# Kernel optimization log

Hardware: AMD Instinct MI355X
Metric: run time of the kernel (lower is better)

## Reference

```python
import jax, jax.numpy as jnp
import numpy as np

HIDDEN = 4096
N_HEADS = 32
N_KV_HEADS = 8
HEAD_DIM = HIDDEN // N_HEADS  # 128
N_GROUPS = N_HEADS // N_KV_HEADS  # 4
ROPE_THETA = 10000.0
NEG_INF = -1e9


def fake_quant(x):
    """Symmetric per-tensor int8 fake quantization (quantize -> dequantize)."""
    scale = jnp.maximum(jnp.max(jnp.abs(x)) / 127.0, 1e-8)
    return jnp.clip(jnp.round(x / scale), -127.0, 127.0) * scale


def q_linear(x, W):
    # torch Linear: y = x @ W.T ; both operands fake-quantized (dequant-inline GEMM)
    return jnp.einsum('bsh,oh->bso', fake_quant(x), fake_quant(W))


def rope_cos_sin(position_ids, head_dim, dtype):
    inv_freq = 1.0 / (ROPE_THETA ** (jnp.arange(0, head_dim, 2, dtype=jnp.float32) / head_dim))
    freqs = position_ids.astype(jnp.float32)[..., None] * inv_freq  # [b, s, hd/2]
    emb = jnp.concatenate([freqs, freqs], axis=-1)                   # [b, s, hd]
    return jnp.cos(emb).astype(dtype), jnp.sin(emb).astype(dtype)


def rotate_half(x):
    x1, x2 = jnp.split(x, 2, axis=-1)
    return jnp.concatenate([-x2, x1], axis=-1)


def setup_inputs() -> dict:
    key = jax.random.key(0)
    ks = jax.random.split(key, 6)
    b, s = 2, 1024
    hidden_states = jax.random.normal(ks[0], (b, s, HIDDEN), dtype=jnp.float32)
    # additive causal mask [b, 1, q, kv]
    causal = jnp.where(jnp.tril(jnp.ones((s, s), dtype=bool)), 0.0, NEG_INF).astype(jnp.float32)
    attention_mask = jnp.broadcast_to(causal[None, None], (b, 1, s, s))
    position_ids = jnp.broadcast_to(jnp.arange(s, dtype=jnp.int64)[None, :], (b, s))
    winit = 1.0 / np.sqrt(HIDDEN)
    Wq = jax.random.normal(ks[1], (HIDDEN, HIDDEN), dtype=jnp.float32) * winit
    Wk = jax.random.normal(ks[2], (N_KV_HEADS * HEAD_DIM, HIDDEN), dtype=jnp.float32) * winit
    Wv = jax.random.normal(ks[3], (N_KV_HEADS * HEAD_DIM, HIDDEN), dtype=jnp.float32) * winit
    Wo = jax.random.normal(ks[4], (HIDDEN, HIDDEN), dtype=jnp.float32) * winit
    return {"hidden_states": hidden_states, "attention_mask": attention_mask,
            "position_ids": position_ids, "Wq": Wq, "Wk": Wk, "Wv": Wv, "Wo": Wo}


def reference(hidden_states, attention_mask, position_ids, Wq, Wk, Wv, Wo):
    b, s, _ = hidden_states.shape
    dtype = hidden_states.dtype

    # quantized QKV projections
    q = q_linear(hidden_states, Wq).reshape(b, s, N_HEADS, HEAD_DIM).transpose(0, 2, 1, 3)
    k = q_linear(hidden_states, Wk).reshape(b, s, N_KV_HEADS, HEAD_DIM).transpose(0, 2, 1, 3)
    v = q_linear(hidden_states, Wv).reshape(b, s, N_KV_HEADS, HEAD_DIM).transpose(0, 2, 1, 3)

    # RoPE
    cos, sin = rope_cos_sin(position_ids, HEAD_DIM, dtype)  # [b, s, hd]
    cos, sin = cos[:, None], sin[:, None]                   # broadcast over heads
    q = q * cos + rotate_half(q) * sin
    k = k * cos + rotate_half(k) * sin

    # GQA: repeat kv heads
    k = jnp.repeat(k, N_GROUPS, axis=1)  # [b, H, s, hd]
    v = jnp.repeat(v, N_GROUPS, axis=1)

    # quantized QK^T (per-tensor fake quant on both operands)
    attn = jnp.einsum('bhqd,bhkd->bhqk', fake_quant(q), fake_quant(k)) / jnp.sqrt(
        jnp.asarray(HEAD_DIM, dtype=jnp.float32)).astype(dtype)
    attn = attn + attention_mask
    attn = jax.nn.softmax(attn.astype(jnp.float32), axis=-1).astype(dtype)
    # attention_dropout = 0.0 (inference)

    # quantized AV matmul
    out = jnp.einsum('bhqk,bhkd->bhqd', fake_quant(attn), fake_quant(v))
    out = out.transpose(0, 2, 1, 3).reshape(b, s, HIDDEN)
    out = q_linear(out, Wo)
    return out
```

## Files before the change

kernel.cpp:

```cpp
#include <hip/hip_runtime.h>
#include <math.h>

#define B_ 2
#define S_ 1024
#define HID 4096
#define NH 32
#define NKV 8
#define HD 128
#define LOG2E 1.44269504088896340736f

typedef short s16x8 __attribute__((ext_vector_type(8)));
typedef float f32x4 __attribute__((ext_vector_type(4)));
typedef unsigned short u16;
typedef u16 u16x4 __attribute__((ext_vector_type(4)));

__device__ __forceinline__ f32x4 mfma16(s16x8 a, s16x8 b, f32x4 c) {
  return __builtin_amdgcn_mfma_f32_16x16x32_bf16(a, b, c, 0, 0, 0);
}
__device__ __forceinline__ u16 f2bf(float f) {
  union { float f; unsigned u; } v; v.f = f;
  return (u16)(v.u >> 16);
}
__device__ __forceinline__ float get_scale(const unsigned* sc, int slot) {
  return fmaxf(__uint_as_float(sc[slot]) / 127.0f, 1e-8f);
}
__device__ __forceinline__ void gload16(const void* g, void* l) {
  __builtin_amdgcn_global_load_lds(
      (const __attribute__((address_space(1))) unsigned*)g,
      (__attribute__((address_space(3))) unsigned*)l, 16, 0, 0);
}
__device__ __forceinline__ void atomic_absmax(unsigned* out, float m, int lane) {
  #pragma unroll
  for (int o = 32; o >= 1; o >>= 1) m = fmaxf(m, __shfl_xor(m, o));
  if (lane == 0) atomicMax(out, __float_as_uint(m));
}

#define SB_() __builtin_amdgcn_sched_barrier(0)
#define PBAR() do { SB_(); __builtin_amdgcn_s_barrier(); SB_(); } while (0)
#define VM6() do { SB_(); asm volatile("s_waitcnt vmcnt(6)" ::: "memory"); } while (0)
#define VM0() do { SB_(); asm volatile("s_waitcnt vmcnt(0)" ::: "memory"); } while (0)

__global__ void absmax5_k(const float4* __restrict__ p0, const float4* __restrict__ p1,
                          const float4* __restrict__ p2, const float4* __restrict__ p3,
                          const float4* __restrict__ p4, unsigned* __restrict__ sc) {
  int r = blockIdx.y;
  const float4* x; int n4;
  if (r == 0)      { x = p0; n4 = B_ * S_ * HID / 4; }
  else if (r == 1) { x = p1; n4 = HID * HID / 4; }
  else if (r == 2) { x = p2; n4 = NKV * HD * HID / 4; }
  else if (r == 3) { x = p3; n4 = NKV * HD * HID / 4; }
  else             { x = p4; n4 = HID * HID / 4; }
  float m = 0.f;
  int stride = gridDim.x * blockDim.x;
  for (int i = blockIdx.x * blockDim.x + threadIdx.x; i < n4; i += stride) {
    float4 v = x[i];
    m = fmaxf(m, fmaxf(fmaxf(fabsf(v.x), fabsf(v.y)), fmaxf(fabsf(v.z), fabsf(v.w))));
  }
  atomic_absmax(sc + r, m, threadIdx.x & 63);
}

__global__ void quant5_k(const float4* __restrict__ p0, const float4* __restrict__ p1,
                         const float4* __restrict__ p2, const float4* __restrict__ p3,
                         const float4* __restrict__ p4,
                         u16x4* __restrict__ y0, u16x4* __restrict__ y1,
                         u16x4* __restrict__ y2, u16x4* __restrict__ y3,
                         u16x4* __restrict__ y4, const unsigned* __restrict__ sc) {
  int r = blockIdx.y;
  const float4* x; u16x4* y; int n4;
  if (r == 0)      { x = p0; y = y0; n4 = B_ * S_ * HID / 4; }
  else if (r == 1) { x = p1; y = y1; n4 = HID * HID / 4; }
  else if (r == 2) { x = p2; y = y2; n4 = NKV * HD * HID / 4; }
  else if (r == 3) { x = p3; y = y3; n4 = NKV * HD * HID / 4; }
  else             { x = p4; y = y4; n4 = HID * HID / 4; }
  float s = get_scale(sc, r);
  int stride = gridDim.x * blockDim.x;
  for (int i = blockIdx.x * blockDim.x + threadIdx.x; i < n4; i += stride) {
    float4 v = x[i];
    u16x4 o;
    o[0] = f2bf(fminf(fmaxf(rintf(v.x / s), -127.f), 127.f));
    o[1] = f2bf(fminf(fmaxf(rintf(v.y / s), -127.f), 127.f));
    o[2] = f2bf(fminf(fmaxf(rintf(v.z / s), -127.f), 127.f));
    o[3] = f2bf(fminf(fmaxf(rintf(v.w / s), -127.f), 127.f));
    y[i] = o;
  }
}

__global__ void quant_k(const float4* __restrict__ x, u16x4* __restrict__ y, int n4,
                        const unsigned* __restrict__ sc, int slot) {
  float s = get_scale(sc, slot);
  int stride = gridDim.x * blockDim.x;
  for (int i = blockIdx.x * blockDim.x + threadIdx.x; i < n4; i += stride) {
    float4 v = x[i];
    u16x4 o;
    o[0] = f2bf(fminf(fmaxf(rintf(v.x / s), -127.f), 127.f));
    o[1] = f2bf(fminf(fmaxf(rintf(v.y / s), -127.f), 127.f));
    o[2] = f2bf(fminf(fmaxf(rintf(v.z / s), -127.f), 127.f));
    o[3] = f2bf(fminf(fmaxf(rintf(v.w / s), -127.f), 127.f));
    y[i] = o;
  }
}

__global__ void add_k(const float4* __restrict__ p0, const float4* __restrict__ p1,
                      float4* __restrict__ out, int n4) {
  int stride = gridDim.x * blockDim.x;
  for (int i = blockIdx.x * blockDim.x + threadIdx.x; i < n4; i += stride) {
    float4 a = p0[i], b = p1[i];
    out[i] = make_float4(a.x + b.x, a.y + b.y, a.z + b.z, a.w + b.w);
  }
}

__device__ __forceinline__ void rdA(const u16* slot, int wm, int lr, int lg,
                                    s16x8 af[4][2]) {
  #pragma unroll
  for (int mi = 0; mi < 4; ++mi) {
    int row = wm * 64 + mi * 16 + lr;
    const char* base = (const char*)slot + row * 128;
    int sw = (row & 7) << 4;
    #pragma unroll
    for (int ks = 0; ks < 2; ++ks)
      af[mi][ks] = *(const s16x8*)(base + ((ks * 64 + lg * 16) ^ sw));
  }
}
__device__ __forceinline__ void rdB(const u16* slot, int wn, int lr, int lg,
                                    s16x8 bf[2][2]) {
  #pragma unroll
  for (int ni = 0; ni < 2; ++ni) {
    int row = wn * 32 + ni * 16 + lr;
    const char* base = (const char*)slot + row * 128;
    int sw = (row & 7) << 4;
    #pragma unroll
    for (int ks = 0; ks < 2; ++ks)
      bf[ni][ks] = *(const s16x8*)(base + ((ks * 64 + lg * 16) ^ sw));
  }
}
template <int PM, int PN>
__device__ __forceinline__ void mfma_phase(f32x4 (&acc)[2][2][4][2],
                                           const s16x8 (&af)[4][2],
                                           const s16x8 (&bf)[2][2]) {
  __builtin_amdgcn_s_setprio(1);
  #pragma unroll
  for (int mi = 0; mi < 4; ++mi)
    #pragma unroll
    for (int ni = 0; ni < 2; ++ni)
      #pragma unroll
      for (int ks = 0; ks < 2; ++ks)
        acc[PM][PN][mi][ni] = mfma16(af[mi][ks], bf[ni][ks], acc[PM][PN][mi][ni]);
  __builtin_amdgcn_s_setprio(0);
}

__device__ void gemm256(const u16* __restrict__ A, const u16* __restrict__ Bm,
                        float* __restrict__ C, int Ncols, int m0, int n0,
                        int k0, int nkt, float scale, unsigned* omax, u16* S) {
  const int tid = threadIdx.x;
  const int wave = tid >> 6, lane = tid & 63;
  const int lr = lane & 15, lg = lane >> 4;
  const int wm = wave >> 2, wn = wave & 3;
  u16* SA00 = S;          u16* SA01 = S + 8192;
  u16* SB00 = S + 16384;  u16* SB01 = S + 24576;
  u16* SA10 = S + 32768;  u16* SA11 = S + 40960;
  u16* SB10 = S + 49152;  u16* SB11 = S + 57344;
  const int r0 = tid >> 3;
  const int ce = (((tid & 7) * 16) ^ ((r0 & 7) << 4)) >> 1;
  const u16* pa0 = A + (size_t)(m0 + r0) * HID + k0 + ce;
  const u16* pa1 = pa0 + (size_t)128 * HID;
  const u16* pb0 = Bm + (size_t)(n0 + r0) * HID + k0 + ce;
  const u16* pb1 = pb0 + (size_t)128 * HID;
  const int wdst = wave * 512;
  f32x4 acc[2][2][4][2] = {};
  s16x8 af[4][2], bf[2][2];

  auto STG = [&](const u16* p, u16* slot, int tcol) {
    const u16* g = p + tcol * 64;
    gload16(g, slot + wdst);
    gload16(g + (size_t)64 * HID, slot + 4096 + wdst);
  };

  STG(pa0, SA00, 0); STG(pb0, SB00, 0); STG(pa1, SA01, 0); STG(pb1, SB01, 0);
  STG(pa0, SA10, 1); STG(pb1, SB11, 1); STG(pa1, SA11, 1);
  VM6(); PBAR();

  #pragma unroll 1
  for (int t = 0; t < nkt; t += 2) {
    const bool g2 = t + 2 < nkt, g3 = t + 3 < nkt;
    rdA(SA00, wm, lr, lg, af); rdB(SB00, wn, lr, lg, bf);
    STG(pb0, SB10, t + 1);
    PBAR(); mfma_phase<0, 0>(acc, af, bf); PBAR();
    rdB(SB01, wn, lr, lg, bf);
    if (g2) STG(pa0, SA00, t + 2);
    PBAR(); mfma_phase<0, 1>(acc, af, bf); PBAR();
    rdA(SA01, wm, lr, lg, af);
    if (g2) STG(pb1, SB01, t + 2);
    PBAR(); mfma_phase<1, 1>(acc, af, bf); PBAR();
    rdB(SB00, wn, lr, lg, bf);
    if (g2) STG(pa1, SA01, t + 2);
    PBAR(); mfma_phase<1, 0>(acc, af, bf);
    if (g2) { VM6(); } else { VM0(); }
    PBAR();
    rdA(SA10, wm, lr, lg, af); rdB(SB10, wn, lr, lg, bf);
    if (g2) STG(pb0, SB00, t + 2);
    PBAR(); mfma_phase<0, 0>(acc, af, bf); PBAR();
    rdB(SB11, wn, lr, lg, bf);
    if (g3) STG(pa0, SA10, t + 3);
    PBAR(); mfma_phase<0, 1>(acc, af, bf); PBAR();
    rdA(SA11, wm, lr, lg, af);
    if (g3) STG(pb1, SB11, t + 3);
    PBAR(); mfma_phase<1, 1>(acc, af, bf); PBAR();
    rdB(SB10, wn, lr, lg, bf);
    if (g3) STG(pa1, SA11, t + 3);
    PBAR(); mfma_phase<1, 0>(acc, af, bf); VM6(); PBAR();
  }

  float gm = 0.f;
  #pragma unroll
  for (int mh = 0; mh < 2; ++mh)
    #pragma unroll
    for (int nh = 0; nh < 2; ++nh)
      #pragma unroll
      for (int mi = 0; mi < 4; ++mi)
        #pragma unroll
        for (int ni = 0; ni < 2; ++ni) {
          size_t rbase = (size_t)(m0 + mh * 128 + wm * 64 + mi * 16 + lg * 4);
          int cb = n0 + nh * 128 + wn * 32 + ni * 16 + lr;
          #pragma unroll
          for (int r = 0; r < 4; ++r) {
            float v = acc[mh][nh][mi][ni][r] * scale;
            gm = fmaxf(gm, fabsf(v));
            C[(rbase + r) * (size_t)Ncols + cb] = v;
          }
        }
  if (omax) atomic_absmax(omax, gm, lane);
}

__global__ __launch_bounds__(512, 1) void gemm_qkv8(
    const u16* __restrict__ Xq, const u16* __restrict__ Wqb,
    const u16* __restrict__ Wkb, const u16* __restrict__ Wvb,
    float* __restrict__ qf, float* __restrict__ kf, float* __restrict__ vf,
    const unsigned* __restrict__ sc, unsigned* __restrict__ vmax) {
  extern __shared__ __align__(16) u16 S[];
  int raw = blockIdx.x;
  int wg = (raw & 7) * 24 + (raw >> 3);
  int bx = wg & 7, by = wg >> 3;
  const u16* Bm; float* C; int Ncols, n0, sslot; unsigned* om = nullptr;
  if (by < 16)      { Bm = Wqb; C = qf; Ncols = HID;      n0 = by * 256;        sslot = 1; }
  else if (by < 20) { Bm = Wkb; C = kf; Ncols = NKV * HD; n0 = (by - 16) * 256; sslot = 2; }
  else              { Bm = Wvb; C = vf; Ncols = NKV * HD; n0 = (by - 20) * 256; sslot = 3; om = vmax; }
  float scale = get_scale(sc, 0) * get_scale(sc, sslot);
  gemm256(Xq, Bm, C, Ncols, bx * 256, n0, 0, 64, scale, om, S);
}

__global__ __launch_bounds__(512, 1) void gemm_o8(
    const u16* __restrict__ A, const u16* __restrict__ Bm,
    float* __restrict__ P0, float* __restrict__ P1,
    const unsigned* __restrict__ sc) {
  extern __shared__ __align__(16) u16 S[];
  int raw = blockIdx.x;
  int wg = (raw & 7) * 32 + (raw >> 3);
  int tile = wg >> 1, half = wg & 1;
  int by = tile & 15, bx = tile >> 4;
  float scale = get_scale(sc, 8) * get_scale(sc, 4);
  gemm256(A, Bm, half ? P1 : P0, HID, bx * 256, by * 256, half * 2048, 32,
          scale, nullptr, S);
}

__global__ void rope_tab_k(float2* __restrict__ tab) {
  int i = blockIdx.x * 256 + threadIdx.x;
  int pos = i >> 6, d = i & 63;
  float inv = exp2f((float)d * (-13.287712379549449f / 64.0f));
  float ang = (float)pos * inv;
  tab[i] = make_float2(cosf(ang), sinf(ang));
}

__global__ void rope2_k(float* __restrict__ qf, float* __restrict__ kf,
                        unsigned* __restrict__ sc, const float2* __restrict__ tab) {
  int reg = blockIdx.y;
  float* q = reg ? kf : qf;
  int nheads = reg ? NKV : NH;
  unsigned* om = sc + (reg ? 6 : 5);
  int total = B_ * S_ * nheads * 64;
  int stride = gridDim.x * blockDim.x;
  float m = 0.f;
  for (int i = blockIdx.x * blockDim.x + threadIdx.x; i < total; i += stride) {
    int d = i & 63;
    int h = (i >> 6) % nheads;
    int bs = i / (64 * nheads);
    int pos = bs & (S_ - 1);
    float2 cs = tab[(pos << 6) + d];
    size_t base = ((size_t)bs * nheads + h) * HD + d;
    float x1 = q[base], x2 = q[base + 64];
    float o1 = x1 * cs.x - x2 * cs.y;
    float o2 = x2 * cs.x + x1 * cs.y;
    q[base] = o1; q[base + 64] = o2;
    m = fmaxf(m, fmaxf(fabsf(o1), fabsf(o2)));
  }
  atomic_absmax(om, m, threadIdx.x & 63);
}

__global__ void quantqk_k(const float4* __restrict__ qf, const float4* __restrict__ kf,
                          u16x4* __restrict__ qq, u16x4* __restrict__ kq,
                          const unsigned* __restrict__ sc) {
  int reg = blockIdx.y;
  const float4* x = reg ? kf : qf;
  u16x4* y = reg ? kq : qq;
  int n4 = reg ? (B_ * S_ * NKV * HD / 4) : (B_ * S_ * HID / 4);
  float s = get_scale(sc, reg ? 6 : 5);
  int stride = gridDim.x * blockDim.x;
  for (int i = blockIdx.x * blockDim.x + threadIdx.x; i < n4; i += stride) {
    float4 v = x[i];
    u16x4 o;
    o[0] = f2bf(fminf(fmaxf(rintf(v.x / s), -127.f), 127.f));
    o[1] = f2bf(fminf(fmaxf(rintf(v.y / s), -127.f), 127.f));
    o[2] = f2bf(fminf(fmaxf(rintf(v.z / s), -127.f), 127.f));
    o[3] = f2bf(fminf(fmaxf(rintf(v.w / s), -127.f), 127.f));
    y[i] = o;
  }
}

__global__ __launch_bounds__(256) void vquant_t_k(const float* __restrict__ vf,
                                                  unsigned* __restrict__ vtw,
                                                  const unsigned* __restrict__ sc) {
  __shared__ u16 Ls[64 * 132];
  float s = get_scale(sc, 7);
  int st = blockIdx.x & 15, kvh = (blockIdx.x >> 4) & 7, b = blockIdx.x >> 7;
  int s0 = st * 64;
  #pragma unroll
  for (int i = 0; i < 8; ++i) {
    int o = i * 256 + threadIdx.x;
    int sr = o >> 5, c4 = o & 31;
    float4 v = *(const float4*)(vf + ((size_t)(b * S_ + s0 + sr)) * (NKV * HD) +
                                kvh * HD + c4 * 4);
    u16x4 w;
    w[0] = f2bf(fminf(fmaxf(rintf(v.x / s), -127.f), 127.f));
    w[1] = f2bf(fminf(fmaxf(rintf(v.y / s), -127.f), 127.f));
    w[2] = f2bf(fminf(fmaxf(rintf(v.z / s), -127.f), 127.f));
    w[3] = f2bf(fminf(fmaxf(rintf(v.w / s), -127.f), 127.f));
    *(u16x4*)(Ls + sr * 132 + c4 * 4) = w;
  }
  __syncthreads();
  #pragma unroll
  for (int i = 0; i < 16; ++i) {
    int o = i * 256 + threadIdx.x;
    int d = o >> 5, sj = o & 31;
    unsigned lo = Ls[(sj * 2) * 132 + d], hi = Ls[(sj * 2 + 1) * 132 + d];
    vtw[(((size_t)(b * NKV + kvh) * HD + d) << 9) + st * 32 + sj] = lo | (hi << 16);
  }
}

__global__ __launch_bounds__(256) void attn_k(
    const u16* __restrict__ Q, const u16* __restrict__ Kq, const u16* __restrict__ Vt,
    float* __restrict__ O, const unsigned* __restrict__ sc, unsigned* __restrict__ omax) {
  __shared__ __align__(16) u16 Ks[2][64 * 128];
  __shared__ __align__(16) u16 Vs[2][128 * 64];
  __shared__ __align__(16) u16 Ps[64 * 64];
  const int tid = threadIdx.x;
  const int wave = tid >> 6, lane = tid & 63;
  const int lr = lane & 15, lg = lane >> 4;
  const int qp = blockIdx.x & 7;
  const int bh = blockIdx.x >> 3;
  const int h = bh & 31, b = bh >> 5;
  const int kvh = h >> 2;
  const float sq = get_scale(sc, 5), sk = get_scale(sc, 6), sv = get_scale(sc, 7);
  const float c2 = sq * sk * 0.08838834764831845f * LOG2E;
  const float M0 = 32.0f;
  const int k_rin = lane >> 4;
  const int k_cb0 = (lane & 15) * 16;
  const int v_rin = lane >> 3;
  const int v_cb = ((lane & 7) * 16) ^ ((v_rin & 7) << 4);
  float gmax = 0.f;

  auto stageK = [&](int buf, int kt) {
    #pragma unroll
    for (int i = 0; i < 4; ++i) {
      int ch = wave * 4 + i;
      int row = ch * 4 + k_rin;
      int cb = k_cb0 ^ ((row & 7) << 4);
      gload16(Kq + (size_t)(b * S_ + kt * 64 + row) * (NKV * HD) + kvh * HD + (cb >> 1),
              Ks[buf] + ch * 512);
    }
  };
  auto stageV = [&](int buf, int kt) {
    #pragma unroll
    for (int i = 0; i < 4; ++i) {
      int ch = wave * 4 + i;
      int vrow = ch * 8 + v_rin;
      gload16(Vt + ((size_t)(b * NKV + kvh) * HD + vrow) * S_ + kt * 64 + (v_cb >> 1),
              Vs[buf] + ch * 512);
    }
  };

  for (int pi = 0; pi < 2; ++pi) {
    const int qt = pi ? 15 - qp : qp;
    const int q0 = qt * 64;
    s16x8 aq[4];
    {
      const u16* qp_ = Q + (size_t)(b * S_ + q0 + wave * 16 + lr) * HID + h * HD + lg * 8;
      #pragma unroll
      for (int ks = 0; ks < 4; ++ks) aq[ks] = *(const s16x8*)(qp_ + ks * 32);
    }
    float ll[4] = {0.f, 0.f, 0.f, 0.f};

    stageK(0, 0);
    __syncthreads();
    for (int kt = 0; kt <= qt; ++kt) {
      const int p = kt & 1;
      if (kt < qt) stageK(p ^ 1, kt + 1);
      f32x4 sacc[4] = {};
      __builtin_amdgcn_s_setprio(1);
      #pragma unroll
      for (int ks = 0; ks < 4; ++ks)
        #pragma unroll
        for (int n = 0; n < 4; ++n) {
          int row = n * 16 + lr;
          s16x8 bk = *(const s16x8*)((const char*)Ks[p] + row * 256 +
                                     ((ks * 64 + lg * 16) ^ ((row & 7) << 4)));
          sacc[n] = mfma16(aq[ks], bk, sacc[n]);
        }
      __builtin_amdgcn_s_setprio(0);
      if (kt < qt) {
        #pragma unroll
        for (int r = 0; r < 4; ++r)
          #pragma unroll
          for (int n = 0; n < 4; ++n)
            ll[r] += exp2f(fmaf(sacc[n][r], c2, -M0));
      } else {
        #pragma unroll
        for (int r = 0; r < 4; ++r) {
          int qg = q0 + wave * 16 + lg * 4 + r;
          #pragma unroll
          for (int n = 0; n < 4; ++n) {
            int kg = kt * 64 + n * 16 + lr;
            float e = exp2f(fmaf(sacc[n][r], c2, -M0));
            ll[r] += (kg <= qg) ? e : 0.f;
          }
        }
      }
      __syncthreads();
    }
    float bias[4];
    #pragma unroll
    for (int r = 0; r < 4; ++r) {
      float l = ll[r];
      #pragma unroll
      for (int o = 8; o >= 1; o >>= 1) l += __shfl_xor(l, o);
      bias[r] = 6.9886846867721655f - __log2f(l) - M0;
    }

    f32x4 oacc[8] = {};
    stageK(0, 0); stageV(0, 0);
    __syncthreads();
    for (int kt = 0; kt <= qt; ++kt) {
      const int p = kt & 1;
      if (kt < qt) { stageK(p ^ 1, kt + 1); stageV(p ^ 1, kt + 1); }
      f32x4 sacc[4] = {};
      __builtin_amdgcn_s_setprio(1);
      #pragma unroll
      for (int ks = 0; ks < 4; ++ks)
        #pragma unroll
        for (int n = 0; n < 4; ++n) {
          int row = n * 16 + lr;
          s16x8 bk = *(const s16x8*)((const char*)Ks[p] + row * 256 +
                                     ((ks * 64 + lg * 16) ^ ((row & 7) << 4)));
          sacc[n] = mfma16(aq[ks], bk, sacc[n]);
        }
      __builtin_amdgcn_s_setprio(0);
      if (kt < qt) {
        #pragma unroll
        for (int r = 0; r < 4; ++r) {
          int prow = wave * 16 + lg * 4 + r;
          #pragma unroll
          for (int n = 0; n < 4; ++n) {
            float p127 = rintf(exp2f(fmaf(sacc[n][r], c2, bias[r])));
            int col = n * 16 + lr;
            *(u16*)((char*)Ps + prow * 128 + ((col * 2) ^ ((prow & 7) << 4))) = f2bf(p127);
          }
        }
      } else {
        #pragma unroll
        for (int r = 0; r < 4; ++r) {
          int prow = wave * 16 + lg * 4 + r;
          int qg = q0 + prow;
          #pragma unroll
          for (int n = 0; n < 4; ++n) {
            int kg = kt * 64 + n * 16 + lr;
            float a = fmaf(sacc[n][r], c2, bias[r]);
            float p127 = (kg <= qg) ? rintf(exp2f(a)) : 0.f;
            int col = n * 16 + lr;
            *(u16*)((char*)Ps + prow * 128 + ((col * 2) ^ ((prow & 7) << 4))) = f2bf(p127);
          }
        }
      }
      __builtin_amdgcn_s_setprio(1);
      #pragma unroll
      for (int ks = 0; ks < 2; ++ks) {
        int prow = wave * 16 + lr;
        s16x8 ap = *(const s16x8*)((const char*)Ps + prow * 128 +
                                   ((ks * 64 + lg * 16) ^ ((prow & 7) << 4)));
        #pragma unroll
        for (int n = 0; n < 8; ++n) {
          int vrow = n * 16 + lr;
          s16x8 bv = *(const s16x8*)((const char*)Vs[p] + vrow * 128 +
                                     ((ks * 64 + lg * 16) ^ ((vrow & 7) << 4)));
          oacc[n] = mfma16(ap, bv, oacc[n]);
        }
      }
      __builtin_amdgcn_s_setprio(0);
      __syncthreads();
    }
    const float pvs = sv * (1.0f / 127.0f);
    #pragma unroll
    for (int n = 0; n < 8; ++n)
      #pragma unroll
      for (int r = 0; r < 4; ++r) {
        float v = oacc[n][r] * pvs;
        gmax = fmaxf(gmax, fabsf(v));
        O[(size_t)(b * S_ + q0 + wave * 16 + lg * 4 + r) * HID + h * HD + n * 16 + lr] = v;
      }
  }
  atomic_absmax(omax, gmax, lane);
}

extern "C" void kernel_launch(void* const* d_in, const int* in_sizes, int n_in,
                              void* d_out, int out_size, void* d_ws, size_t ws_size,
                              hipStream_t stream) {
  const float* hs = (const float*)d_in[0];
  const float* Wq = (const float*)d_in[3];
  const float* Wk = (const float*)d_in[4];
  const float* Wv = (const float*)d_in[5];
  const float* Wo = (const float*)d_in[6];
  float* out = (float*)d_out;
  char* ws = (char*)d_ws;

  unsigned* sc = (unsigned*)ws;
  size_t off = 256;
  u16* Xq = (u16*)(ws + off); off += (size_t)B_ * S_ * HID * 2;
  size_t wqb_off = off;
  u16* Wqb = (u16*)(ws + off); off += (size_t)HID * HID * 2;
  u16* Wkb = (u16*)(ws + off); off += (size_t)NKV * HD * HID * 2;
  u16* Wvb = (u16*)(ws + off); off += (size_t)NKV * HD * HID * 2;
  u16* Wob = (u16*)(ws + off); off += (size_t)HID * HID * 2;
  size_t qf_off = off;
  float* qf = (float*)(ws + off); off += (size_t)B_ * S_ * HID * 4;
  size_t kf_off = off;
  float* kf = (float*)(ws + off); off += (size_t)B_ * S_ * NKV * HD * 4;
  float* vf = (float*)(ws + off); off += (size_t)B_ * S_ * NKV * HD * 4;
  u16* qq = (u16*)(ws + off); off += (size_t)B_ * S_ * HID * 2;
  u16* kq = (u16*)(ws + off); off += (size_t)B_ * S_ * NKV * HD * 2;
  u16* vt = (u16*)(ws + off); off += (size_t)B_ * S_ * NKV * HD * 2;
  float2* tab = (float2*)(ws + off); off += (size_t)S_ * 64 * 8;
  float* attnf = (float*)(ws + qf_off);
  u16* attnq = (u16*)(ws + wqb_off);
  float* P0 = (float*)(ws + qf_off);
  float* P1 = (float*)(ws + kf_off);

  hipFuncSetAttribute((const void*)gemm_qkv8,
                      hipFuncAttributeMaxDynamicSharedMemorySize, 131072);
  hipFuncSetAttribute((const void*)gemm_o8,
                      hipFuncAttributeMaxDynamicSharedMemorySize, 131072);

  hipMemsetAsync(sc, 0, 64, stream);

  dim3 blk(256);
  absmax5_k<<<dim3(416, 5), blk, 0, stream>>>(
      (const float4*)hs, (const float4*)Wq, (const float4*)Wk,
      (const float4*)Wv, (const float4*)Wo, sc);
  quant5_k<<<dim3(416, 5), blk, 0, stream>>>(
      (const float4*)hs, (const float4*)Wq, (const float4*)Wk,
      (const float4*)Wv, (const float4*)Wo,
      (u16x4*)Xq, (u16x4*)Wqb, (u16x4*)Wkb, (u16x4*)Wvb, (u16x4*)Wob, sc);
  rope_tab_k<<<256, blk, 0, stream>>>(tab);

  gemm_qkv8<<<192, 512, 131072, stream>>>(Xq, Wqb, Wkb, Wvb, qf, kf, vf, sc, sc + 7);

  rope2_k<<<dim3(512, 2), blk, 0, stream>>>(qf, kf, sc, tab);
  quantqk_k<<<dim3(512, 2), blk, 0, stream>>>((const float4*)qf, (const float4*)kf,
                                              (u16x4*)qq, (u16x4*)kq, sc);
  vquant_t_k<<<256, blk, 0, stream>>>(vf, (unsigned*)vt, sc);

  attn_k<<<512, blk, 0, stream>>>(qq, kq, vt, attnf, sc, sc + 8);

  quant_k<<<2048, blk, 0, stream>>>((const float4*)attnf, (u16x4*)attnq,
                                    B_ * S_ * HID / 4, sc, 8);
  gemm_o8<<<256, 512, 131072, stream>>>(attnq, Wob, P0, P1, sc);
  add_k<<<2048, blk, 0, stream>>>((const float4*)P0, (const float4*)P1,
                                  (float4*)out, B_ * S_ * HID / 4);
}
```

Before: 553.5 us.

## Double attention query tile to 128 rows with 8 waves and XCD-aware head mapping

The attention kernel now processes 128-query tiles with 512 threads (8 waves) instead of 64-query tiles with 4 waves, halving the grid to 256 blocks. Each staged K/V tile is therefore reused by twice as many query rows, which cuts global loads and staging work per query. Block indices are also remapped so that the four query heads sharing a KV head, and the same batch/KV group, land on the same XCD for better L2 reuse. The trade-offs are fewer blocks on a large GPU, coarser causal load balancing, and a larger shared-memory footprint for the P buffer.

```diff
diff --git a/kernel.cpp b/kernel.cpp
--- a/kernel.cpp
+++ b/kernel.cpp
@@ -345,19 +345,22 @@
   }
 }
 
-__global__ __launch_bounds__(256) void attn_k(
+__global__ __launch_bounds__(512) void attn_k(
     const u16* __restrict__ Q, const u16* __restrict__ Kq, const u16* __restrict__ Vt,
     float* __restrict__ O, const unsigned* __restrict__ sc, unsigned* __restrict__ omax) {
   __shared__ __align__(16) u16 Ks[2][64 * 128];
   __shared__ __align__(16) u16 Vs[2][128 * 64];
-  __shared__ __align__(16) u16 Ps[64 * 64];
+  __shared__ __align__(16) u16 Ps[128 * 64];
   const int tid = threadIdx.x;
   const int wave = tid >> 6, lane = tid & 63;
   const int lr = lane & 15, lg = lane >> 4;
-  const int qp = blockIdx.x & 7;
-  const int bh = blockIdx.x >> 3;
-  const int h = bh & 31, b = bh >> 5;
-  const int kvh = h >> 2;
+  const int raw = blockIdx.x;
+  const int xcd = raw & 7, j = raw >> 3;
+  const int grp = xcd + 8 * (j >> 4);
+  const int within = j & 15;
+  const int b = grp >> 3, kvh = grp & 7;
+  const int h = kvh * 4 + (within >> 2);
+  const int qp = within & 3;
   const float sq = get_scale(sc, 5), sk = get_scale(sc, 6), sv = get_scale(sc, 7);
   const float c2 = sq * sk * 0.08838834764831845f * LOG2E;
   const float M0 = 32.0f;
@@ -369,8 +372,8 @@
 
   auto stageK = [&](int buf, int kt) {
     #pragma unroll
-    for (int i = 0; i < 4; ++i) {
-      int ch = wave * 4 + i;
+    for (int i = 0; i < 2; ++i) {
+      int ch = wave * 2 + i;
       int row = ch * 4 + k_rin;
       int cb = k_cb0 ^ ((row & 7) << 4);
       gload16(Kq + (size_t)(b * S_ + kt * 64 + row) * (NKV * HD) + kvh * HD + (cb >> 1),
@@ -379,8 +382,8 @@
   };
   auto stageV = [&](int buf, int kt) {
     #pragma unroll
-    for (int i = 0; i < 4; ++i) {
-      int ch = wave * 4 + i;
+    for (int i = 0; i < 2; ++i) {
+      int ch = wave * 2 + i;
       int vrow = ch * 8 + v_rin;
       gload16(Vt + ((size_t)(b * NKV + kvh) * HD + vrow) * S_ + kt * 64 + (v_cb >> 1),
               Vs[buf] + ch * 512);
@@ -388,8 +391,10 @@
   };
 
   for (int pi = 0; pi < 2; ++pi) {
-    const int qt = pi ? 15 - qp : qp;
-    const int q0 = qt * 64;
+    const int qt = pi ? 7 - qp : qp;
+    const int q0 = qt * 128;
+    const int nkt = 2 * (qt + 1);
+    const int qwmin = q0 + wave * 16;
     s16x8 aq[4];
     {
       const u16* qp_ = Q + (size_t)(b * S_ + q0 + wave * 16 + lr) * HID + h * HD + lg * 8;
@@ -400,9 +405,9 @@
 
     stageK(0, 0);
     __syncthreads();
-    for (int kt = 0; kt <= qt; ++kt) {
+    for (int kt = 0; kt < nkt; ++kt) {
       const int p = kt & 1;
-      if (kt < qt) stageK(p ^ 1, kt + 1);
+      if (kt < nkt - 1) stageK(p ^ 1, kt + 1);
       f32x4 sacc[4] = {};
       __builtin_amdgcn_s_setprio(1);
       #pragma unroll
@@ -415,7 +420,7 @@
           sacc[n] = mfma16(aq[ks], bk, sacc[n]);
         }
       __builtin_amdgcn_s_setprio(0);
-      if (kt < qt) {
+      if (kt * 64 + 63 <= qwmin) {
         #pragma unroll
         for (int r = 0; r < 4; ++r)
           #pragma unroll
@@ -424,7 +429,7 @@
       } else {
         #pragma unroll
         for (int r = 0; r < 4; ++r) {
-          int qg = q0 + wave * 16 + lg * 4 + r;
+          int qg = qwmin + lg * 4 + r;
           #pragma unroll
           for (int n = 0; n < 4; ++n) {
             int kg = kt * 64 + n * 16 + lr;
@@ -447,9 +452,9 @@
     f32x4 oacc[8] = {};
     stageK(0, 0); stageV(0, 0);
     __syncthreads();
-    for (int kt = 0; kt <= qt; ++kt) {
+    for (int kt = 0; kt < nkt; ++kt) {
       const int p = kt & 1;
-      if (kt < qt) { stageK(p ^ 1, kt + 1); stageV(p ^ 1, kt + 1); }
+      if (kt < nkt - 1) { stageK(p ^ 1, kt + 1); stageV(p ^ 1, kt + 1); }
       f32x4 sacc[4] = {};
       __builtin_amdgcn_s_setprio(1);
       #pragma unroll
@@ -462,7 +467,7 @@
           sacc[n] = mfma16(aq[ks], bk, sacc[n]);
         }
       __builtin_amdgcn_s_setprio(0);
-      if (kt < qt) {
+      if (kt * 64 + 63 <= qwmin) {
         #pragma unroll
         for (int r = 0; r < 4; ++r) {
           int prow = wave * 16 + lg * 4 + r;
@@ -477,7 +482,7 @@
         #pragma unroll
         for (int r = 0; r < 4; ++r) {
           int prow = wave * 16 + lg * 4 + r;
-          int qg = q0 + prow;
+          int qg = qwmin + lg * 4 + r;
           #pragma unroll
           for (int n = 0; n < 4; ++n) {
             int kg = kt * 64 + n * 16 + lr;
@@ -575,7 +580,7 @@
                                               (u16x4*)qq, (u16x4*)kq, sc);
   vquant_t_k<<<256, blk, 0, stream>>>(vf, (unsigned*)vt, sc);
 
-  attn_k<<<512, blk, 0, stream>>>(qq, kq, vt, attnf, sc, sc + 8);
+  attn_k<<<256, 512, 0, stream>>>(qq, kq, vt, attnf, sc, sc + 8);
 
   quant_k<<<2048, blk, 0, stream>>>((const float4*)attnf, (u16x4*)attnq,
                                     B_ * S_ * HID / 4, sc, 8);
```

Result: no change. 558.0 us (+0.8%).
